# Optimization experiments

Hardware: AMD Instinct MI355X
Metric: run time of the kernel (lower is better)

## Reference

```python
import jax, jax.numpy as jnp
import numpy as np

REWARD_SCALE = 1.0
DIST_NORM = 2
LATENT_DIST_THRESHOLD = 6.0

BS, N_VIEWS, N_PART, F_DIM = 128, 4, 1024, 10


def setup_inputs() -> dict:
    key = jax.random.key(0)
    k1, k2, k3, k4 = jax.random.split(key, 4)
    achieved_goal = jax.random.normal(k1, (BS, N_VIEWS, N_PART, F_DIM), jnp.float32)
    desired_goal = jax.random.normal(k2, (BS, N_VIEWS, N_PART, F_DIM), jnp.float32)
    norm_mean = jax.random.normal(k3, (F_DIM,), jnp.float32)
    norm_std = jax.random.uniform(k4, (F_DIM,), jnp.float32, minval=0.5, maxval=1.5)
    return {"achieved_goal": achieved_goal, "desired_goal": desired_goal,
            "norm_mean": norm_mean, "norm_std": norm_std}


def _pairwise_sqdist(x, y):
    # x: [bs, n, d], y: [bs, m, d] -> [bs, n, m] squared L2 ('l2_simple')
    xx = jnp.sum(x * x, axis=-1)            # [bs, n]
    yy = jnp.sum(y * y, axis=-1)            # [bs, m]
    xy = jnp.einsum('bnd,bmd->bnm', x, y)   # [bs, n, m]
    return xx[:, :, None] + yy[:, None, :] - 2.0 * xy


def _particle_mask(particles):
    # latent_classifier is None -> obj_class_cond = ones -> mask = (1 == 0) = all False
    obj_on = particles[..., -1]
    return jnp.zeros_like(obj_on, dtype=bool)


def reference(achieved_goal, desired_goal, norm_mean, norm_std):
    # unnormalize (particle_normalizer.unnormalize modeled as affine)
    state_particles = achieved_goal * norm_std + norm_mean
    goal_particles = desired_goal * norm_std + norm_mean
    bs, n_views, n_particles, _ = state_particles.shape

    state_mask = _particle_mask(state_particles)   # [bs, nv, np] bool
    goal_mask = _particle_mask(goal_particles)

    # P_mask[b,v,i,j] = state_mask[b,v,i] | goal_mask[b,v,j]
    P_mask = jnp.logical_or(state_mask[..., :, None], goal_mask[..., None, :])

    state_vis = state_particles[..., 5:9]
    state_xy = state_particles[..., :2]
    goal_vis = goal_particles[..., 5:9]
    goal_xy = goal_particles[..., :2]

    inf = jnp.asarray(jnp.inf, state_particles.dtype)
    rewards = []
    for i in range(n_views):
        sxy = state_xy[:, i]                 # [bs, np, 2]
        gxy = goal_xy[:, i]
        gmask_i = goal_mask[:, i]            # [bs, np]
        smask_i = state_mask[:, i]

        P = _pairwise_sqdist(state_vis[:, i], goal_vis[:, i])  # [bs, np_state, np_goal]
        P = jnp.where(P_mask[:, i], inf, P)

        # goal -> state direction: min over state dim (axis 1)
        min_d1 = jnp.min(P, axis=1)                            # [bs, np_goal]
        idx1 = jnp.argmin(P, axis=1)                           # [bs, np_goal]
        d_goal = jnp.take_along_axis(sxy, idx1[..., None], axis=1)  # [bs, np_goal, 2]
        xy_dist_1 = jnp.linalg.norm(gxy - d_goal, ord=DIST_NORM, axis=-1)
        xy_dist_1 = jnp.where(min_d1 > LATENT_DIST_THRESHOLD, 1.0, xy_dist_1)
        xy_dist_1 = jnp.where(gmask_i, 0.0, xy_dist_1)
        n_obj_g = jnp.maximum(jnp.sum(~gmask_i, axis=1), 1)
        reward_g2s = -jnp.sum(xy_dist_1, axis=1) / n_obj_g

        # state -> goal direction: min over goal dim (axis 2)
        min_d2 = jnp.min(P, axis=2)
        idx2 = jnp.argmin(P, axis=2)
        d_state = jnp.take_along_axis(gxy, idx2[..., None], axis=1)
        xy_dist_2 = jnp.linalg.norm(sxy - d_state, ord=DIST_NORM, axis=-1)
        xy_dist_2 = jnp.where(min_d2 > LATENT_DIST_THRESHOLD, 1.0, xy_dist_2)
        xy_dist_2 = jnp.where(smask_i, 0.0, xy_dist_2)
        n_obj_s = jnp.maximum(jnp.sum(~smask_i, axis=1), 1)
        reward_s2g = -jnp.sum(xy_dist_2, axis=1) / n_obj_s

        rv = (reward_g2s + reward_s2g) / 2.0
        no_valid = jnp.logical_or(jnp.all(gmask_i, axis=-1), jnp.all(smask_i, axis=-1))
        rv = jnp.where(no_valid, -1.0, rv)
        rewards.append(rv)

    reward = jnp.mean(jnp.stack(rewards, axis=0), axis=0)   # [bs]
    return REWARD_SCALE * reward[:, None]                    # [bs, 1]
```

## Files before the change

### kernel.cpp

```cpp
#include <hip/hip_runtime.h>
#include <cstdint>
#include <cstddef>

#define NP   1024
#define HALF 512
#define FD   10
#define BSZ  128
#define TPB  256
#define RPT  8

#define PIN(f4) asm volatile("" : "+v"(f4.x), "+v"(f4.y), "+v"(f4.z), "+v"(f4.w))

extern "C" __global__ __launch_bounds__(TPB, 4)
void chamfer_pairs(const float* __restrict__ ag, const float* __restrict__ dg,
                   const float* __restrict__ nmean, const float* __restrict__ nstd,
                   float* __restrict__ out )
{
    __shared__ __align__(16) float4 cvis[NP];
    __shared__ __align__(16) float  csh[NP];
    __shared__ float bD[2 * NP];
    __shared__ int   bI[2 * NP];
    __shared__ float red[TPB / 64];

    const int bid  = blockIdx.x;
    const int pair = bid >> 1;
    const int d    = bid & 1;
    const int tid  = threadIdx.x;
    const int w    = tid >> 6;
    const int lane = tid & 63;
    const int rowhalf = w & 1;
    const int colhalf = w >> 1;
    const int cbase   = colhalf * HALF;

    const float* rowsrc = ((d == 0) ? ag : dg) + (size_t)pair * (NP * FD);
    const float* colsrc = ((d == 0) ? dg : ag) + (size_t)pair * (NP * FD);

    const float s5 = -2.0f * nstd[5], m5 = -2.0f * nmean[5];
    const float s6 = -2.0f * nstd[6], m6 = -2.0f * nmean[6];
    const float s7 = -2.0f * nstd[7], m7 = -2.0f * nmean[7];
    const float s8 = -2.0f * nstd[8], m8 = -2.0f * nmean[8];
    const float std0 = nstd[0], mean0 = nmean[0];
    const float std1 = nstd[1], mean1 = nmean[1];

    for (int m = tid; m < NP; m += TPB) {
        const float* p = colsrc + (size_t)m * FD;
        float t0 = fmaf(p[5], s5, m5);
        float t1 = fmaf(p[6], s6, m6);
        float t2 = fmaf(p[7], s7, m7);
        float t3 = fmaf(p[8], s8, m8);
        cvis[m] = make_float4(t0, t1, t2, t3);
        csh[m]  = 0.25f * (t0 * t0 + t1 * t1 + t2 * t2 + t3 * t3);
    }

    float4 rv[RPT];
    float  bestd[RPT];
    int    bblk[RPT];
#pragma unroll
    for (int r = 0; r < RPT; ++r) {
        int n = rowhalf * HALF + lane + 64 * r;
        const float* p = rowsrc + (size_t)n * FD;
        float t0 = fmaf(p[5], s5, m5);
        float t1 = fmaf(p[6], s6, m6);
        float t2 = fmaf(p[7], s7, m7);
        float t3 = fmaf(p[8], s8, m8);
        rv[r] = make_float4(-0.5f * t0, -0.5f * t1, -0.5f * t2, -0.5f * t3);
        bestd[r] = 3.0e38f;
        bblk[r]  = cbase;
    }
    __syncthreads();

    for (int g = 0; g < HALF / 8; ++g) {
        const int m = cbase + g * 8;
        float4 c0 = cvis[m + 0];
        float4 c1 = cvis[m + 1];
        float4 c2 = cvis[m + 2];
        float4 c3 = cvis[m + 3];
        float4 c4 = cvis[m + 4];
        float4 c5 = cvis[m + 5];
        float4 c6 = cvis[m + 6];
        float4 c7 = cvis[m + 7];
        float4 csA = *(const float4*)(csh + m);
        float4 csB = *(const float4*)(csh + m + 4);
        PIN(c0); PIN(c1); PIN(c2); PIN(c3);
        PIN(c4); PIN(c5); PIN(c6); PIN(c7);
        PIN(csA); PIN(csB);
#pragma unroll
        for (int r = 0; r < RPT; ++r) {
            float4 v = rv[r];
            float d0 = fmaf(v.x, c0.x, csA.x); d0 = fmaf(v.y, c0.y, d0); d0 = fmaf(v.z, c0.z, d0); d0 = fmaf(v.w, c0.w, d0);
            float d1 = fmaf(v.x, c1.x, csA.y); d1 = fmaf(v.y, c1.y, d1); d1 = fmaf(v.z, c1.z, d1); d1 = fmaf(v.w, c1.w, d1);
            float d2 = fmaf(v.x, c2.x, csA.z); d2 = fmaf(v.y, c2.y, d2); d2 = fmaf(v.z, c2.z, d2); d2 = fmaf(v.w, c2.w, d2);
            float d3 = fmaf(v.x, c3.x, csA.w); d3 = fmaf(v.y, c3.y, d3); d3 = fmaf(v.z, c3.z, d3); d3 = fmaf(v.w, c3.w, d3);
            float d4 = fmaf(v.x, c4.x, csB.x); d4 = fmaf(v.y, c4.y, d4); d4 = fmaf(v.z, c4.z, d4); d4 = fmaf(v.w, c4.w, d4);
            float d5 = fmaf(v.x, c5.x, csB.y); d5 = fmaf(v.y, c5.y, d5); d5 = fmaf(v.z, c5.z, d5); d5 = fmaf(v.w, c5.w, d5);
            float d6 = fmaf(v.x, c6.x, csB.z); d6 = fmaf(v.y, c6.y, d6); d6 = fmaf(v.z, c6.z, d6); d6 = fmaf(v.w, c6.w, d6);
            float d7 = fmaf(v.x, c7.x, csB.w); d7 = fmaf(v.y, c7.y, d7); d7 = fmaf(v.z, c7.z, d7); d7 = fmaf(v.w, c7.w, d7);
            float p0 = fminf(fminf(d0, d1), d2);
            float p1 = fminf(fminf(d3, d4), d5);
            float p2 = fminf(d6, d7);
            float bm = fminf(fminf(p0, p1), p2);
            bool lt = bm < bestd[r];
            bestd[r] = fminf(bestd[r], bm);
            bblk[r]  = lt ? m : bblk[r];
        }
    }

#pragma unroll
    for (int r = 0; r < RPT; ++r) {
        int n  = rowhalf * HALF + lane + 64 * r;
        int mb = bblk[r];
        float4 v = rv[r];
        float dd[8];
#pragma unroll
        for (int j = 0; j < 8; ++j) {
            float4 c = cvis[mb + j];
            float cs = csh[mb + j];
            float t = fmaf(v.x, c.x, cs);
            t = fmaf(v.y, c.y, t);
            t = fmaf(v.z, c.z, t);
            t = fmaf(v.w, c.w, t);
            dd[j] = t;
        }
        int sel = 0;
#pragma unroll
        for (int j = 7; j >= 0; --j)
            if (dd[j] == bestd[r]) sel = j;
        bD[colhalf * NP + n] = bestd[r];
        bI[colhalf * NP + n] = mb + sel;
    }
    __syncthreads();

    float sum = 0.0f;
#pragma unroll
    for (int r = 0; r < 4; ++r) {
        int n = tid + TPB * r;
        float d0v = bD[n], d1v = bD[NP + n];
        int   i0 = bI[n], i1 = bI[NP + n];
        bool h1 = d1v < d0v;
        float bd = h1 ? d1v : d0v;
        int   bi = h1 ? i1 : i0;

        const float* p = rowsrc + (size_t)n * FD;
        float t0 = fmaf(p[5], s5, m5);
        float t1 = fmaf(p[6], s6, m6);
        float t2 = fmaf(p[7], s7, m7);
        float t3 = fmaf(p[8], s8, m8);
        float rss = 0.25f * (t0 * t0 + t1 * t1 + t2 * t2 + t3 * t3);

        const float* pc = colsrc + (size_t)bi * FD;
        float gx = fmaf(pc[0], std0, mean0);
        float gy = fmaf(pc[1], std1, mean1);
        float ax = fmaf(p[0], std0, mean0);
        float ay = fmaf(p[1], std1, mean1);
        float dx = ax - gx;
        float dy = ay - gy;
        float dist = sqrtf(dx * dx + dy * dy);
        if (bd > 6.0f - rss) dist = 1.0f;
        sum += dist;
    }

    for (int o = 32; o > 0; o >>= 1) sum += __shfl_down(sum, o, 64);
    if (lane == 0) red[w] = sum;
    __syncthreads();
    if (tid == 0) {
        float s = red[0] + red[1] + red[2] + red[3];
        atomicAdd(&out[bid >> 3], s * (-1.0f / 8192.0f));
    }
}

extern "C" void kernel_launch(void* const* d_in, const int* in_sizes, int n_in,
                              void* d_out, int out_size, void* d_ws, size_t ws_size,
                              hipStream_t stream)
{
    const float* ag = (const float*)d_in[0];
    const float* dg = (const float*)d_in[1];
    const float* nm = (const float*)d_in[2];
    const float* ns = (const float*)d_in[3];

    hipMemsetAsync(d_out, 0, BSZ * sizeof(float), stream);
    chamfer_pairs<<<BSZ * 4 * 2, TPB, 0, stream>>>(ag, dg, nm, ns, (float*)d_out);
}
```

Measured before the change: 212.9 us.

## Halve block size, double rows per thread, double-buffer column batches

Blocks shrink from 256 to 128 threads. Each wave now covers all 1024 rows, 16 per thread, against one half of the columns, so every column value loaded from shared memory is reused across twice as many rows. The inner loop double-buffers the shared-memory column batches to overlap loads with the FMA chain. The argmin refinement recomputes candidate features from global memory instead of shared memory. Register pressure rises sharply and fewer waves are resident, which may hurt latency hiding.

```diff
diff --git a/kernel.cpp b/kernel.cpp
--- a/kernel.cpp
+++ b/kernel.cpp
@@ -6,12 +6,30 @@
 #define HALF 512
 #define FD   10
 #define BSZ  128
-#define TPB  256
-#define RPT  8
+#define TPB  128
+#define RPT  16
 
 #define PIN(f4) asm volatile("" : "+v"(f4.x), "+v"(f4.y), "+v"(f4.z), "+v"(f4.w))
 
-extern "C" __global__ __launch_bounds__(TPB, 4)
+__device__ __forceinline__ void stage_one(const float* __restrict__ p,
+                                          float s5, float m5, float s6, float m6,
+                                          float s7, float m7, float s8, float m8,
+                                          float4& t, float& cs)
+{
+    t.x = fmaf(p[5], s5, m5);
+    t.y = fmaf(p[6], s6, m6);
+    t.z = fmaf(p[7], s7, m7);
+    t.w = fmaf(p[8], s8, m8);
+    float a = t.x * t.x;
+    a = fmaf(t.y, t.y, a);
+    a = fmaf(t.z, t.z, a);
+    a = fmaf(t.w, t.w, a);
+    cs = 0.25f * a;
+}
+
+struct Batch { float4 c[8]; float4 sA, sB; };
+
+extern "C" __global__ __launch_bounds__(TPB, 2)
 void chamfer_pairs(const float* __restrict__ ag, const float* __restrict__ dg,
                    const float* __restrict__ nmean, const float* __restrict__ nstd,
                    float* __restrict__ out )
@@ -20,17 +38,15 @@
     __shared__ __align__(16) float  csh[NP];
     __shared__ float bD[2 * NP];
     __shared__ int   bI[2 * NP];
-    __shared__ float red[TPB / 64];
+    __shared__ float red[2];
 
     const int bid  = blockIdx.x;
+    const int d    = bid & 1;
     const int pair = bid >> 1;
-    const int d    = bid & 1;
     const int tid  = threadIdx.x;
     const int w    = tid >> 6;
     const int lane = tid & 63;
-    const int rowhalf = w & 1;
-    const int colhalf = w >> 1;
-    const int cbase   = colhalf * HALF;
+    const int cbase = w * HALF;
 
     const float* rowsrc = ((d == 0) ? ag : dg) + (size_t)pair * (NP * FD);
     const float* colsrc = ((d == 0) ? dg : ag) + (size_t)pair * (NP * FD);
@@ -43,13 +59,10 @@
     const float std1 = nstd[1], mean1 = nmean[1];
 
     for (int m = tid; m < NP; m += TPB) {
-        const float* p = colsrc + (size_t)m * FD;
-        float t0 = fmaf(p[5], s5, m5);
-        float t1 = fmaf(p[6], s6, m6);
-        float t2 = fmaf(p[7], s7, m7);
-        float t3 = fmaf(p[8], s8, m8);
-        cvis[m] = make_float4(t0, t1, t2, t3);
-        csh[m]  = 0.25f * (t0 * t0 + t1 * t1 + t2 * t2 + t3 * t3);
+        float4 t; float cs;
+        stage_one(colsrc + (size_t)m * FD, s5, m5, s6, m6, s7, m7, s8, m8, t, cs);
+        cvis[m] = t;
+        csh[m]  = cs;
     }
 
     float4 rv[RPT];
@@ -57,44 +70,38 @@
     int    bblk[RPT];
 #pragma unroll
     for (int r = 0; r < RPT; ++r) {
-        int n = rowhalf * HALF + lane + 64 * r;
-        const float* p = rowsrc + (size_t)n * FD;
-        float t0 = fmaf(p[5], s5, m5);
-        float t1 = fmaf(p[6], s6, m6);
-        float t2 = fmaf(p[7], s7, m7);
-        float t3 = fmaf(p[8], s8, m8);
-        rv[r] = make_float4(-0.5f * t0, -0.5f * t1, -0.5f * t2, -0.5f * t3);
+        int n = lane + 64 * r;
+        float4 t; float cs;
+        stage_one(rowsrc + (size_t)n * FD, s5, m5, s6, m6, s7, m7, s8, m8, t, cs);
+        rv[r] = make_float4(-0.5f * t.x, -0.5f * t.y, -0.5f * t.z, -0.5f * t.w);
         bestd[r] = 3.0e38f;
         bblk[r]  = cbase;
     }
     __syncthreads();
 
-    for (int g = 0; g < HALF / 8; ++g) {
+    auto loadb = [&](int g, Batch& b) {
+        const int m = cbase + (g & (HALF / 8 - 1)) * 8;
+#pragma unroll
+        for (int j = 0; j < 8; ++j) b.c[j] = cvis[m + j];
+        b.sA = *(const float4*)(csh + m);
+        b.sB = *(const float4*)(csh + m + 4);
+#pragma unroll
+        for (int j = 0; j < 8; ++j) PIN(b.c[j]);
+        PIN(b.sA); PIN(b.sB);
+    };
+    auto computeb = [&](const Batch& b, int g) {
         const int m = cbase + g * 8;
-        float4 c0 = cvis[m + 0];
-        float4 c1 = cvis[m + 1];
-        float4 c2 = cvis[m + 2];
-        float4 c3 = cvis[m + 3];
-        float4 c4 = cvis[m + 4];
-        float4 c5 = cvis[m + 5];
-        float4 c6 = cvis[m + 6];
-        float4 c7 = cvis[m + 7];
-        float4 csA = *(const float4*)(csh + m);
-        float4 csB = *(const float4*)(csh + m + 4);
-        PIN(c0); PIN(c1); PIN(c2); PIN(c3);
-        PIN(c4); PIN(c5); PIN(c6); PIN(c7);
-        PIN(csA); PIN(csB);
 #pragma unroll
         for (int r = 0; r < RPT; ++r) {
             float4 v = rv[r];
-            float d0 = fmaf(v.x, c0.x, csA.x); d0 = fmaf(v.y, c0.y, d0); d0 = fmaf(v.z, c0.z, d0); d0 = fmaf(v.w, c0.w, d0);
-            float d1 = fmaf(v.x, c1.x, csA.y); d1 = fmaf(v.y, c1.y, d1); d1 = fmaf(v.z, c1.z, d1); d1 = fmaf(v.w, c1.w, d1);
-            float d2 = fmaf(v.x, c2.x, csA.z); d2 = fmaf(v.y, c2.y, d2); d2 = fmaf(v.z, c2.z, d2); d2 = fmaf(v.w, c2.w, d2);
-            float d3 = fmaf(v.x, c3.x, csA.w); d3 = fmaf(v.y, c3.y, d3); d3 = fmaf(v.z, c3.z, d3); d3 = fmaf(v.w, c3.w, d3);
-            float d4 = fmaf(v.x, c4.x, csB.x); d4 = fmaf(v.y, c4.y, d4); d4 = fmaf(v.z, c4.z, d4); d4 = fmaf(v.w, c4.w, d4);
-            float d5 = fmaf(v.x, c5.x, csB.y); d5 = fmaf(v.y, c5.y, d5); d5 = fmaf(v.z, c5.z, d5); d5 = fmaf(v.w, c5.w, d5);
-            float d6 = fmaf(v.x, c6.x, csB.z); d6 = fmaf(v.y, c6.y, d6); d6 = fmaf(v.z, c6.z, d6); d6 = fmaf(v.w, c6.w, d6);
-            float d7 = fmaf(v.x, c7.x, csB.w); d7 = fmaf(v.y, c7.y, d7); d7 = fmaf(v.z, c7.z, d7); d7 = fmaf(v.w, c7.w, d7);
+            float d0 = fmaf(v.x, b.c[0].x, b.sA.x); d0 = fmaf(v.y, b.c[0].y, d0); d0 = fmaf(v.z, b.c[0].z, d0); d0 = fmaf(v.w, b.c[0].w, d0);
+            float d1 = fmaf(v.x, b.c[1].x, b.sA.y); d1 = fmaf(v.y, b.c[1].y, d1); d1 = fmaf(v.z, b.c[1].z, d1); d1 = fmaf(v.w, b.c[1].w, d1);
+            float d2 = fmaf(v.x, b.c[2].x, b.sA.z); d2 = fmaf(v.y, b.c[2].y, d2); d2 = fmaf(v.z, b.c[2].z, d2); d2 = fmaf(v.w, b.c[2].w, d2);
+            float d3 = fmaf(v.x, b.c[3].x, b.sA.w); d3 = fmaf(v.y, b.c[3].y, d3); d3 = fmaf(v.z, b.c[3].z, d3); d3 = fmaf(v.w, b.c[3].w, d3);
+            float d4 = fmaf(v.x, b.c[4].x, b.sB.x); d4 = fmaf(v.y, b.c[4].y, d4); d4 = fmaf(v.z, b.c[4].z, d4); d4 = fmaf(v.w, b.c[4].w, d4);
+            float d5 = fmaf(v.x, b.c[5].x, b.sB.y); d5 = fmaf(v.y, b.c[5].y, d5); d5 = fmaf(v.z, b.c[5].z, d5); d5 = fmaf(v.w, b.c[5].w, d5);
+            float d6 = fmaf(v.x, b.c[6].x, b.sB.z); d6 = fmaf(v.y, b.c[6].y, d6); d6 = fmaf(v.z, b.c[6].z, d6); d6 = fmaf(v.w, b.c[6].w, d6);
+            float d7 = fmaf(v.x, b.c[7].x, b.sB.w); d7 = fmaf(v.y, b.c[7].y, d7); d7 = fmaf(v.z, b.c[7].z, d7); d7 = fmaf(v.w, b.c[7].w, d7);
             float p0 = fminf(fminf(d0, d1), d2);
             float p1 = fminf(fminf(d3, d4), d5);
             float p2 = fminf(d6, d7);
@@ -103,36 +110,45 @@
             bestd[r] = fminf(bestd[r], bm);
             bblk[r]  = lt ? m : bblk[r];
         }
+    };
+
+    Batch A, B;
+    loadb(0, A);
+    for (int g = 0; g < HALF / 8; g += 2) {
+        loadb(g + 1, B);
+        computeb(A, g);
+        loadb(g + 2, A);
+        computeb(B, g + 1);
     }
 
 #pragma unroll
     for (int r = 0; r < RPT; ++r) {
-        int n  = rowhalf * HALF + lane + 64 * r;
+        int n  = lane + 64 * r;
         int mb = bblk[r];
         float4 v = rv[r];
         float dd[8];
 #pragma unroll
         for (int j = 0; j < 8; ++j) {
-            float4 c = cvis[mb + j];
-            float cs = csh[mb + j];
-            float t = fmaf(v.x, c.x, cs);
-            t = fmaf(v.y, c.y, t);
-            t = fmaf(v.z, c.z, t);
-            t = fmaf(v.w, c.w, t);
-            dd[j] = t;
+            float4 t; float cs;
+            stage_one(colsrc + (size_t)(mb + j) * FD, s5, m5, s6, m6, s7, m7, s8, m8, t, cs);
+            float u = fmaf(v.x, t.x, cs);
+            u = fmaf(v.y, t.y, u);
+            u = fmaf(v.z, t.z, u);
+            u = fmaf(v.w, t.w, u);
+            dd[j] = u;
         }
         int sel = 0;
 #pragma unroll
         for (int j = 7; j >= 0; --j)
             if (dd[j] == bestd[r]) sel = j;
-        bD[colhalf * NP + n] = bestd[r];
-        bI[colhalf * NP + n] = mb + sel;
+        bD[w * NP + n] = bestd[r];
+        bI[w * NP + n] = mb + sel;
     }
     __syncthreads();
 
     float sum = 0.0f;
 #pragma unroll
-    for (int r = 0; r < 4; ++r) {
+    for (int r = 0; r < 8; ++r) {
         int n = tid + TPB * r;
         float d0v = bD[n], d1v = bD[NP + n];
         int   i0 = bI[n], i1 = bI[NP + n];
@@ -141,11 +157,8 @@
         int   bi = h1 ? i1 : i0;
 
         const float* p = rowsrc + (size_t)n * FD;
-        float t0 = fmaf(p[5], s5, m5);
-        float t1 = fmaf(p[6], s6, m6);
-        float t2 = fmaf(p[7], s7, m7);
-        float t3 = fmaf(p[8], s8, m8);
-        float rss = 0.25f * (t0 * t0 + t1 * t1 + t2 * t2 + t3 * t3);
+        float4 t; float rss;
+        stage_one(p, s5, m5, s6, m6, s7, m7, s8, m8, t, rss);
 
         const float* pc = colsrc + (size_t)bi * FD;
         float gx = fmaf(pc[0], std0, mean0);
@@ -163,7 +176,7 @@
     if (lane == 0) red[w] = sum;
     __syncthreads();
     if (tid == 0) {
-        float s = red[0] + red[1] + red[2] + red[3];
+        float s = red[0] + red[1];
         atomicAdd(&out[bid >> 3], s * (-1.0f / 8192.0f));
     }
 }
```

New measurement: 210.3 us. About the same (-1.2%).
